# Kernel optimization log

Measured on AMD Instinct MI355X. Metric: run time of the kernel, lower is better.

## Reference

```python
import jax, jax.numpy as jnp
import numpy as np

GRID_SIZE = 5
SPLINE_ORDER = 3

def _grid():
    h = 2.0 / GRID_SIZE
    return jnp.arange(-SPLINE_ORDER, GRID_SIZE + SPLINE_ORDER + 1, dtype=jnp.float32) * h - 1.0

def b_splines(x):
    # x: (..., in) -> (..., in, GRID_SIZE + SPLINE_ORDER) Cox-de Boor bases on uniform grid [-1,1]
    g = _grid()
    x = x[..., None]
    bases = ((x >= g[:-1]) & (x < g[1:])).astype(x.dtype)
    for k in range(1, SPLINE_ORDER + 1):
        bases = ((x - g[:-(k + 1)]) / (g[k:-1] - g[:-(k + 1)]) * bases[..., :-1]
                 + (g[k + 1:] - x) / (g[k + 1:] - g[1:-k]) * bases[..., 1:])
    return bases

def kan(x, base_w, spline_w):
    # efficient-KAN KANLinear: silu(x) @ Wb^T + Bspline(x) contracted with Ws
    base = jax.nn.silu(x) @ base_w.T
    return base + jnp.einsum('...ik,oik->...o', b_splines(x), spline_w)

def token_mixing(X, ln_w, ln_b, k1b, k1s, k2b, k2s, eps=1e-5):
    # X: (B, C, L); LayerNorm over [L, C] jointly after permute, then KAN over last (token) dim
    z = jnp.transpose(X, (0, 2, 1))  # (B, L, C)
    mu = z.mean(axis=(-2, -1), keepdims=True)
    var = ((z - mu) ** 2).mean(axis=(-2, -1), keepdims=True)
    z = (z - mu) / jnp.sqrt(var + eps) * ln_w + ln_b
    z = jnp.transpose(z, (0, 2, 1))
    z = kan(z, k1b, k1s)
    z = kan(z, k2b, k2s)
    return X + z

def prob_distance(X, A):
    # Mahalanobis_mask.calculate_prob_distance
    XF = jnp.abs(jnp.fft.rfft(X, axis=-1))           # (B, C, F)
    diff = XF[:, :, None, :] - XF[:, None, :, :]     # (B, C, C, F)
    temp = jnp.einsum('dk,bxck->bxcd', A, diff)
    dist = jnp.einsum('bxcd,bxcd->bxc', temp, temp)
    exp_dist = 1.0 / (dist + 1e-10)
    C = exp_dist.shape[-1]
    eye = jnp.eye(C, dtype=exp_dist.dtype)
    off = 1.0 - eye
    exp_dist = exp_dist * off
    exp_max = jax.lax.stop_gradient(jnp.max(exp_dist, axis=-1, keepdims=True))
    p = exp_dist / exp_max
    return (p * off + eye) * 0.99

def gcn_spatial(x, a, w, b):
    # nconv spatial: einsum('bld,blw->bld', x, A) == x * A.sum(-1, keepdims); order=2, eval-mode dropout=identity
    s = jnp.sum(a, axis=-1, keepdims=True)  # (B, C, 1)
    x1 = x * s
    x2 = x1 * s
    h = jnp.concatenate([x, x1, x2], axis=-1) @ w.T + b
    return jax.nn.gelu(h, approximate=False)  # torch nn.GELU (erf)

def _forward(x, tm1_ln_w, tm1_ln_b, tm1_k1_base, tm1_k1_spline, tm1_k2_base, tm1_k2_spline, A1, g1_w, g1_b,
             k1_base, k1_spline, tm_ln_w, tm_ln_b, tm_k1_base, tm_k1_spline, tm_k2_base, tm_k2_spline, A2,
             g2_w, g2_b, k2_base, k2_spline):
    tm1 = token_mixing(x, tm1_ln_w, tm1_ln_b, tm1_k1_base, tm1_k1_spline, tm1_k2_base, tm1_k2_spline)
    P1 = prob_distance(tm1, A1)
    y1 = gcn_spatial(tm1, jax.nn.softmax(P1, axis=-1), g1_w, g1_b)
    cm = kan(x, k1_base, k1_spline)              # (B, C4, D)
    tm = token_mixing(cm, tm_ln_w, tm_ln_b, tm_k1_base, tm_k1_spline, tm_k2_base, tm_k2_spline)
    P3 = prob_distance(tm, A2)
    y2 = gcn_spatial(tm, jax.nn.softmax(P3, axis=-1), g2_w, g2_b)
    z = kan(y2, k2_base, k2_spline)              # (B, C4, T)
    return y1 + z

def setup_inputs() -> dict:
    key = jax.random.key(0)
    ks = jax.random.split(key, 20)
    B, T, D, C4, H, K = 16, 512, 512, 128, 64, GRID_SIZE + SPLINE_ORDER
    FT, FD = T // 2 + 1, D // 2 + 1
    r = lambda k, shape, s=0.05: jax.random.normal(k, shape, dtype=jnp.float32) * s
    return {
        'x': jax.random.normal(ks[0], (B, C4, T), dtype=jnp.float32),
        'tm1_ln_w': jnp.ones((T, C4), jnp.float32),
        'tm1_ln_b': jnp.zeros((T, C4), jnp.float32),
        'tm1_k1_base': r(ks[1], (H, T)),
        'tm1_k1_spline': r(ks[2], (H, T, K)),
        'tm1_k2_base': r(ks[3], (T, H)),
        'tm1_k2_spline': r(ks[4], (T, H, K)),
        'A1': jax.random.normal(ks[5], (FT, FT), dtype=jnp.float32),
        'g1_w': r(ks[6], (T, 3 * T), 0.02),
        'g1_b': jnp.zeros((T,), jnp.float32),
        'k1_base': r(ks[7], (D, T)),
        'k1_spline': r(ks[8], (D, T, K)),
        'tm_ln_w': jnp.ones((D, C4), jnp.float32),
        'tm_ln_b': jnp.zeros((D, C4), jnp.float32),
        'tm_k1_base': r(ks[9], (H, D)),
        'tm_k1_spline': r(ks[10], (H, D, K)),
        'tm_k2_base': r(ks[11], (D, H)),
        'tm_k2_spline': r(ks[12], (D, H, K)),
        'A2': jax.random.normal(ks[13], (FD, FD), dtype=jnp.float32),
        'g2_w': r(ks[14], (D, 3 * D), 0.02),
        'g2_b': jnp.zeros((D,), jnp.float32),
        'k2_base': r(ks[15], (T, D)),
        'k2_spline': r(ks[16], (T, D, K)),
    }

def reference(x, tm1_ln_w, tm1_ln_b, tm1_k1_base, tm1_k1_spline, tm1_k2_base, tm1_k2_spline, A1, g1_w, g1_b,
              k1_base, k1_spline, tm_ln_w, tm_ln_b, tm_k1_base, tm_k1_spline, tm_k2_base, tm_k2_spline, A2,
              g2_w, g2_b, k2_base, k2_spline):
    return _forward(x, tm1_ln_w, tm1_ln_b, tm1_k1_base, tm1_k1_spline, tm1_k2_base, tm1_k2_spline, A1, g1_w, g1_b,
                    k1_base, k1_spline, tm_ln_w, tm_ln_b, tm_k1_base, tm_k1_spline, tm_k2_base, tm_k2_spline, A2,
                    g2_w, g2_b, k2_base, k2_spline)
```

## Files before the change

### kernel.cpp

```cpp
#include <hip/hip_runtime.h>
#include <hip/hip_bf16.h>


#define M_ROWS 2048
#define TDIM   512
#define C4DIM  128
#define NFEAT  9
#define HZ     12
#define BZ     4

typedef unsigned short u16;
typedef __attribute__((ext_vector_type(8))) short short8;
typedef __attribute__((ext_vector_type(4))) float f32x4;

__device__ __forceinline__ float bf2f(u16 u) {
    union { unsigned int i; float f; } c; c.i = ((unsigned int)u) << 16; return c.f;
}
__device__ __forceinline__ u16 f2bf(float v) {
    __hip_bfloat16 h = __float2bfloat16(v);
    return *reinterpret_cast<u16*>(&h);
}
__device__ __forceinline__ float siluf(float v) { return v / (1.0f + __expf(-v)); }
__device__ __forceinline__ float geluf(float v) {
    return 0.5f * v * (1.0f + erff(v * 0.70710678118654752440f));
}
__device__ __forceinline__ void gload16(const void* g, void* l) {
    __builtin_amdgcn_global_load_lds(
        (const __attribute__((address_space(1))) unsigned int*)g,
        (__attribute__((address_space(3))) unsigned int*)l, 16, 0, 0);
}

__device__ __forceinline__ void features9(float v, float* f) {
    f[0] = siluf(v);
    float b[11];
#pragma unroll
    for (int i = 0; i < 11; ++i) {
        float gi  = (float)(i - 3) * 0.4f - 1.0f;
        float gi1 = (float)(i - 2) * 0.4f - 1.0f;
        b[i] = (v >= gi && v < gi1) ? 1.0f : 0.0f;
    }
#pragma unroll
    for (int k = 1; k <= 3; ++k) {
#pragma unroll
        for (int i = 0; i + k < 11; ++i) {
            float gi   = (float)(i - 3) * 0.4f - 1.0f;
            float gi1  = (float)(i - 2) * 0.4f - 1.0f;
            float gik  = (float)(i + k - 3) * 0.4f - 1.0f;
            float gik1 = (float)(i + k - 2) * 0.4f - 1.0f;
            b[i] = (v - gi) * (1.0f / (gik - gi)) * b[i]
                 + (gik1 - v) * (1.0f / (gik1 - gi1)) * b[i + 1];
        }
    }
#pragma unroll
    for (int k = 0; k < 8; ++k) f[1 + k] = b[k];
}

struct PrepPtrs {
    const float *g1_w, *g2_w;
    const float *b1, *s1, *b2, *s2, *b3, *s3, *b4, *s4, *b5, *s5, *b6, *s6;
    u16 *WE1, *WE2, *W1a, *W1b, *W2a, *W2b, *KX1, *KX2;
    const float *ln1w, *ln1b, *ln2w, *ln2b;
    float *LNT;
    float *SR;
};

__device__ __forceinline__ void wcat_one(const float* bw, const float* sw, u16* out,
                                         int idx, int I) {
    int o = idx / I, i = idx - o * I;
    u16* w = out + (size_t)o * NFEAT * I;
    w[i] = f2bf(bw[idx]);
    const float* sp = sw + (size_t)idx * 8;
#pragma unroll
    for (int k = 0; k < 8; ++k) w[(1 + k) * I + i] = f2bf(sp[k]);
}

__global__ void prep_all(PrepPtrs p) {
    int blk = blockIdx.x, tid = threadIdx.x;
    if (blk < 2048) {
        const float* gw = blk < 1024 ? p.g1_w : p.g2_w;
        u16* we = blk < 1024 ? p.WE1 : p.WE2;
        int idx = (blk & 1023) * 256 + tid;
        int o = idx >> 9, i = idx & 511;
        const float* r = gw + (size_t)o * 1536;
        we[idx] = f2bf(r[i] + r[512 + i] + r[1024 + i]);
    } else if (blk < 2560) {
        int sub = blk - 2048, which = sub >> 7;
        int idx = (sub & 127) * 256 + tid;
        if (which == 0)      wcat_one(p.b1, p.s1, p.W1a, idx, 512);
        else if (which == 1) wcat_one(p.b2, p.s2, p.W1b, idx, 512);
        else if (which == 2) wcat_one(p.b3, p.s3, p.W2a, idx, 64);
        else                 wcat_one(p.b4, p.s4, p.W2b, idx, 64);
    } else if (blk < 4608) {
        int sub = blk - 2560;
        int idx = (sub & 1023) * 256 + tid;
        if (sub < 1024) wcat_one(p.b5, p.s5, p.KX1, idx, 512);
        else            wcat_one(p.b6, p.s6, p.KX2, idx, 512);
    } else if (blk < 5632) {
        int sub = blk - 4608, which = sub >> 8;
        const float* src = which == 0 ? p.ln1w : which == 1 ? p.ln1b
                         : which == 2 ? p.ln2w : p.ln2b;
        float* dst = p.LNT + (size_t)which * 65536;
        int idx = (sub & 255) * 256 + tid;
        int c = idx & 127, l = idx >> 7;
        dst[c * 512 + l] = src[idx];
    } else {
        if (tid < 64) p.SR[tid] = 0.f;
    }
}

__global__ void stats1_convert(const float* __restrict__ X, u16* __restrict__ XB,
                               float* __restrict__ SR) {
    int idx = (blockIdx.x * 256 + threadIdx.x) * 4;
    float4 v = *reinterpret_cast<const float4*>(X + idx);
    ushort4 o; o.x = f2bf(v.x); o.y = f2bf(v.y); o.z = f2bf(v.z); o.w = f2bf(v.w);
    *reinterpret_cast<ushort4*>(XB + idx) = o;
    float s = v.x + v.y + v.z + v.w;
    float q = v.x * v.x + v.y * v.y + v.z * v.z + v.w * v.w;
#pragma unroll
    for (int off = 32; off > 0; off >>= 1) {
        s += __shfl_down(s, off);
        q += __shfl_down(q, off);
    }
    __shared__ float ls[4], lq[4];
    int wv = threadIdx.x >> 6;
    if ((threadIdx.x & 63) == 0) { ls[wv] = s; lq[wv] = q; }
    __syncthreads();
    if (threadIdx.x == 0) {
        s = ls[0] + ls[1] + ls[2] + ls[3];
        q = lq[0] + lq[1] + lq[2] + lq[3];
        int b = (blockIdx.x * 1024) >> 16;
        atomicAdd(&SR[b * 2], s);
        atomicAdd(&SR[b * 2 + 1], q);
    }
}

__global__ void reduce4_bf16_stats(const float* __restrict__ P, u16* __restrict__ out,
                                   float* __restrict__ SR) {
    int idx = (blockIdx.x * 256 + threadIdx.x) * 4;
    const size_t PL = (size_t)M_ROWS * 512;
    float4 sv = *reinterpret_cast<const float4*>(P + idx);
#pragma unroll
    for (int z = 1; z < BZ; ++z) {
        float4 t = *reinterpret_cast<const float4*>(P + z * PL + idx);
        sv.x += t.x; sv.y += t.y; sv.z += t.z; sv.w += t.w;
    }
    ushort4 o; o.x = f2bf(sv.x); o.y = f2bf(sv.y); o.z = f2bf(sv.z); o.w = f2bf(sv.w);
    *reinterpret_cast<ushort4*>(out + idx) = o;
    float s = sv.x + sv.y + sv.z + sv.w;
    float q = sv.x * sv.x + sv.y * sv.y + sv.z * sv.z + sv.w * sv.w;
#pragma unroll
    for (int off = 32; off > 0; off >>= 1) {
        s += __shfl_down(s, off);
        q += __shfl_down(q, off);
    }
    __shared__ float ls[4], lq[4];
    int wv = threadIdx.x >> 6;
    if ((threadIdx.x & 63) == 0) { ls[wv] = s; lq[wv] = q; }
    __syncthreads();
    if (threadIdx.x == 0) {
        s = ls[0] + ls[1] + ls[2] + ls[3];
        q = lq[0] + lq[1] + lq[2] + lq[3];
        int b = (blockIdx.x * 1024) >> 16;
        atomicAdd(&SR[b * 2], s);
        atomicAdd(&SR[b * 2 + 1], q);
    }
}


__global__ void build_feat_dual(const float* __restrict__ X, const float* __restrict__ SR,
                                const float* __restrict__ lnwT, const float* __restrict__ lnbT,
                                u16* __restrict__ FA, u16* __restrict__ FB) {
    int m = blockIdx.x;
    int i0 = threadIdx.x * 4;
    float4 xv = *reinterpret_cast<const float4*>(X + (size_t)m * TDIM + i0);
    int b = m >> 7, c = m & 127;
    float mu   = SR[b * 2] * (1.0f / 65536.0f);
    float var  = SR[b * 2 + 1] * (1.0f / 65536.0f) - mu * mu;
    float rstd = rsqrtf(var + 1e-5f);
    float4 lw = *reinterpret_cast<const float4*>(lnwT + (size_t)c * 512 + i0);
    float4 lb = *reinterpret_cast<const float4*>(lnbT + (size_t)c * 512 + i0);
    float fb[4][NFEAT], fa[4][NFEAT];
    float xe[4] = {xv.x, xv.y, xv.z, xv.w};
    float lwv[4] = {lw.x, lw.y, lw.z, lw.w};
    float lbv[4] = {lb.x, lb.y, lb.z, lb.w};
#pragma unroll
    for (int e = 0; e < 4; ++e) {
        features9(xe[e], fb[e]);
        features9((xe[e] - mu) * rstd * lwv[e] + lbv[e], fa[e]);
    }
    u16* oa = FA + (size_t)m * (NFEAT * TDIM) + i0;
    u16* ob = FB + (size_t)m * (NFEAT * TDIM) + i0;
#pragma unroll
    for (int j = 0; j < NFEAT; ++j) {
        ushort4 va, vb;
        va.x = f2bf(fa[0][j]); va.y = f2bf(fa[1][j]);
        va.z = f2bf(fa[2][j]); va.w = f2bf(fa[3][j]);
        vb.x = f2bf(fb[0][j]); vb.y = f2bf(fb[1][j]);
        vb.z = f2bf(fb[2][j]); vb.w = f2bf(fb[3][j]);
        *reinterpret_cast<ushort4*>(oa + j * TDIM) = va;
        *reinterpret_cast<ushort4*>(ob + j * TDIM) = vb;
    }
}

__global__ void build_feat_ln(const u16* __restrict__ X, const float* __restrict__ SR,
                              const float* __restrict__ lnwT, const float* __restrict__ lnbT,
                              u16* __restrict__ FA) {
    int m = blockIdx.x;
    int i0 = threadIdx.x * 4;
    ushort4 xu = *reinterpret_cast<const ushort4*>(X + (size_t)m * TDIM + i0);
    int b = m >> 7, c = m & 127;
    float mu   = SR[b * 2] * (1.0f / 65536.0f);
    float var  = SR[b * 2 + 1] * (1.0f / 65536.0f) - mu * mu;
    float rstd = rsqrtf(var + 1e-5f);
    float4 lw = *reinterpret_cast<const float4*>(lnwT + (size_t)c * 512 + i0);
    float4 lb = *reinterpret_cast<const float4*>(lnbT + (size_t)c * 512 + i0);
    float fa[4][NFEAT];
    float xe[4] = {bf2f(xu.x), bf2f(xu.y), bf2f(xu.z), bf2f(xu.w)};
    float lwv[4] = {lw.x, lw.y, lw.z, lw.w};
    float lbv[4] = {lb.x, lb.y, lb.z, lb.w};
#pragma unroll
    for (int e = 0; e < 4; ++e)
        features9((xe[e] - mu) * rstd * lwv[e] + lbv[e], fa[e]);
    u16* oa = FA + (size_t)m * (NFEAT * TDIM) + i0;
#pragma unroll
    for (int j = 0; j < NFEAT; ++j) {
        ushort4 va;
        va.x = f2bf(fa[0][j]); va.y = f2bf(fa[1][j]);
        va.z = f2bf(fa[2][j]); va.w = f2bf(fa[3][j]);
        *reinterpret_cast<ushort4*>(oa + j * TDIM) = va;
    }
}

__global__ void build_feat2(const float* __restrict__ PART, u16* __restrict__ FEAT2) {
    int idx = blockIdx.x * blockDim.x + threadIdx.x;
    int m = idx >> 6, i = idx & 63;
    float h = 0.f;
#pragma unroll
    for (int z = 0; z < HZ; ++z) h += PART[((size_t)z * M_ROWS + m) * 64 + i];
    float f[NFEAT];
    features9(h, f);
    u16* out = FEAT2 + (size_t)m * (NFEAT * 64) + i;
#pragma unroll
    for (int j = 0; j < NFEAT; ++j) out[j * 64] = f2bf(f[j]);
}

__global__ void reduce4_add(const float* __restrict__ P, float* __restrict__ out) {
    int idx = (blockIdx.x * 256 + threadIdx.x) * 4;
    const size_t PL = (size_t)M_ROWS * 512;
    float4 s = *reinterpret_cast<float4*>(out + idx);
#pragma unroll
    for (int z = 0; z < BZ; ++z) {
        float4 t = *reinterpret_cast<const float4*>(P + z * PL + idx);
        s.x += t.x; s.y += t.y; s.z += t.z; s.w += t.w;
    }
    *reinterpret_cast<float4*>(out + idx) = s;
}

__global__ __launch_bounds__(512)
void gemm_big(const u16* __restrict__ A, const u16* __restrict__ B,
              float* __restrict__ Cout) {
    constexpr int Kd = 4608, kPerZ = Kd / BZ, NT = 512;
    constexpr int nt = kPerZ / 64;
    __shared__ u16 As[2][64][64];
    __shared__ u16 Bs[2][128][64];

    const int lin = blockIdx.x;
    const int sw  = (lin & 7) * 64 + (lin >> 3);
    const int bn = (sw & 3) * 128;
    const int bm = ((sw >> 2) & 31) * 64;
    const int z  = sw >> 7;

    const int tid  = threadIdx.x;
    const int wave = tid >> 6, lane = tid & 63;
    const int wm = (wave >> 2) * 32, wn = (wave & 3) * 32;
    const int lr = lane & 15, kh = lane >> 4;

    const u16* Ab = A + (size_t)bm * Kd + z * kPerZ;
    const u16* Bb = B + (size_t)bn * Kd + z * kPerZ;

    const int l3  = lane >> 3;
    const int swz = ((lane & 7) ^ l3) * 8;

    f32x4 acc[2][2];
#pragma unroll
    for (int a = 0; a < 2; ++a)
#pragma unroll
        for (int b = 0; b < 2; ++b) acc[a][b] = (f32x4){0.f, 0.f, 0.f, 0.f};

#define BIG_ISSUE(buf, kt)                                                         \
    {                                                                              \
        _Pragma("unroll")                                                          \
        for (int c = 0; c < 3; ++c) {                                              \
            int cc = wave * 3 + c;                                                 \
            if (cc < 8) {                                                          \
                int row = cc * 8 + l3;                                             \
                gload16(Ab + (size_t)row * Kd + (kt) + swz, &As[buf][cc * 8][0]);  \
            } else {                                                               \
                int row = (cc - 8) * 8 + l3;                                       \
                gload16(Bb + (size_t)row * Kd + (kt) + swz, &Bs[buf][(cc - 8) * 8][0]); \
            }                                                                      \
        }                                                                          \
    }

    BIG_ISSUE(0, 0);
    int cur = 0;
    for (int t = 0; t < nt; ++t) {
        __syncthreads();
        if (t + 1 < nt) BIG_ISSUE(cur ^ 1, (t + 1) * 64);
#pragma unroll
        for (int ks = 0; ks < 2; ++ks) {
            short8 af[2], bfr[2];
#pragma unroll
            for (int a = 0; a < 2; ++a) {
                int row = wm + a * 16 + lr;
                af[a] = *reinterpret_cast<const short8*>(
                    &As[cur][row][((ks * 4 + kh) ^ (lr & 7)) * 8]);
            }
#pragma unroll
            for (int b = 0; b < 2; ++b) {
                int row = wn + b * 16 + lr;
                bfr[b] = *reinterpret_cast<const short8*>(
                    &Bs[cur][row][((ks * 4 + kh) ^ (lr & 7)) * 8]);
            }
#pragma unroll
            for (int a = 0; a < 2; ++a)
#pragma unroll
                for (int b = 0; b < 2; ++b)
                    acc[a][b] = __builtin_amdgcn_mfma_f32_16x16x32_bf16(af[a], bfr[b], acc[a][b], 0, 0, 0);
        }
        cur ^= 1;
    }

    const int r0 = kh * 4;
#pragma unroll
    for (int a = 0; a < 2; ++a)
#pragma unroll
        for (int b = 0; b < 2; ++b)
#pragma unroll
            for (int r = 0; r < 4; ++r) {
                int row = bm + wm + a * 16 + r0 + r;
                int col = bn + wn + b * 16 + lr;
                Cout[((size_t)z * M_ROWS + row) * NT + col] = acc[a][b][r];
            }
}

template<int BM, int BN, int EPI, bool OUTF32>
__global__ __launch_bounds__(256)
void gemm_mfma(const u16* __restrict__ A, const u16* __restrict__ B,
               void* __restrict__ Cout, const void* __restrict__ aux,
               int M, int N, int Kd, int kPerZ) {
    constexpr int WSM = BM / 2, WSN = BN / 2;
    constexpr int FM = WSM / 16, FN = WSN / 16;
    constexpr int CA = BM / 32, CB = BN / 32;
    __shared__ u16 As[BM][72];
    __shared__ u16 Bs[BN][72];

    const int tid  = threadIdx.x;
    const int wave = tid >> 6, lane = tid & 63;
    const int wm = (wave >> 1) * WSM, wn = (wave & 1) * WSN;
    const int lr = lane & 15, kh = lane >> 4;
    const int bm = blockIdx.y * BM, bn = blockIdx.x * BN;
    const int k0 = blockIdx.z * kPerZ;
    const int nt = kPerZ >> 6;

    const u16* Ab = A + (size_t)bm * Kd + k0;
    const u16* Bb = B + (size_t)bn * Kd + k0;

    f32x4 acc[FM][FN];
#pragma unroll
    for (int a = 0; a < FM; ++a)
#pragma unroll
        for (int b = 0; b < FN; ++b) acc[a][b] = (f32x4){0.f, 0.f, 0.f, 0.f};

    uint4 arA[CA], brA[CB], arB[CA], brB[CB];

#define GLOADT(ar, br, kt)                                                          \
    {                                                                               \
        _Pragma("unroll")                                                           \
        for (int c = 0; c < CA; ++c) {                                              \
            int id = tid + c * 256;                                                 \
            ar[c] = *reinterpret_cast<const uint4*>(Ab + (size_t)(id >> 3) * Kd + (kt) + (id & 7) * 8); \
        }                                                                           \
        _Pragma("unroll")                                                           \
        for (int c = 0; c < CB; ++c) {                                              \
            int id = tid + c * 256;                                                 \
            br[c] = *reinterpret_cast<const uint4*>(Bb + (size_t)(id >> 3) * Kd + (kt) + (id & 7) * 8); \
        }                                                                           \
    }
#define GWRITET(ar, br)                                                             \
    {                                                                               \
        _Pragma("unroll")                                                           \
        for (int c = 0; c < CA; ++c) {                                              \
            int id = tid + c * 256;                                                 \
            *reinterpret_cast<uint4*>(&As[id >> 3][(id & 7) * 8]) = ar[c];          \
        }                                                                           \
        _Pragma("unroll")                                                           \
        for (int c = 0; c < CB; ++c) {                                              \
            int id = tid + c * 256;                                                 \
            *reinterpret_cast<uint4*>(&Bs[id >> 3][(id & 7) * 8]) = br[c];          \
        }                                                                           \
    }
#define GMFMAT()                                                                    \
    {                                                                               \
        _Pragma("unroll")                                                           \
        for (int ks = 0; ks < 2; ++ks) {                                            \
            short8 af[FM], bfr[FN];                                                 \
            _Pragma("unroll")                                                       \
            for (int a = 0; a < FM; ++a)                                            \
                af[a] = *reinterpret_cast<const short8*>(&As[wm + a * 16 + lr][ks * 32 + kh * 8]); \
            _Pragma("unroll")                                                       \
            for (int b = 0; b < FN; ++b)                                            \
                bfr[b] = *reinterpret_cast<const short8*>(&Bs[wn + b * 16 + lr][ks * 32 + kh * 8]); \
            _Pragma("unroll")                                                       \
            for (int a = 0; a < FM; ++a)                                            \
                _Pragma("unroll")                                                   \
                for (int b = 0; b < FN; ++b)                                        \
                    acc[a][b] = __builtin_amdgcn_mfma_f32_16x16x32_bf16(af[a], bfr[b], acc[a][b], 0, 0, 0); \
        }                                                                           \
    }

    GLOADT(arA, brA, 0);
    if (nt > 1) GLOADT(arB, brB, 64);
    int t = 0;
    for (; t + 1 < nt; t += 2) {
        __syncthreads();
        GWRITET(arA, brA);
        __syncthreads();
        if (t + 2 < nt) GLOADT(arA, brA, (t + 2) * 64);
        GMFMAT();
        __syncthreads();
        GWRITET(arB, brB);
        __syncthreads();
        if (t + 3 < nt) GLOADT(arB, brB, (t + 3) * 64);
        GMFMAT();
    }
    if (t < nt) {
        __syncthreads();
        GWRITET(arA, brA);
        __syncthreads();
        GMFMAT();
    }

    const int r0 = kh * 4;
#pragma unroll
    for (int a = 0; a < FM; ++a) {
#pragma unroll
        for (int b = 0; b < FN; ++b) {
#pragma unroll
            for (int r = 0; r < 4; ++r) {
                int row = bm + wm + a * 16 + r0 + r;
                int col = bn + wn + b * 16 + lr;
                float v = acc[a][b][r];
                if (EPI == 0) {
                    ((float*)Cout)[((size_t)blockIdx.z * M + row) * N + col] = v;
                } else if (EPI == 1) {
                    v += bf2f(((const u16*)aux)[(size_t)row * N + col]);
                    ((u16*)Cout)[(size_t)row * N + col] = f2bf(v);
                } else if (EPI == 2) {
                    v = geluf(v + ((const float*)aux)[col]);
                    if (OUTF32) ((float*)Cout)[(size_t)row * N + col] = v;
                    else        ((u16*)Cout)[(size_t)row * N + col] = f2bf(v);
                } else {
                    v = geluf(v + ((const float*)aux)[col]);
                    float f[NFEAT];
                    features9(v, f);
                    u16* o = (u16*)Cout + (size_t)row * (NFEAT * TDIM) + col;
#pragma unroll
                    for (int j = 0; j < NFEAT; ++j) o[j * TDIM] = f2bf(f[j]);
                }
            }
        }
    }
}

extern "C" void kernel_launch(void* const* d_in, const int* in_sizes, int n_in,
                              void* d_out, int out_size, void* d_ws, size_t ws_size,
                              hipStream_t stream) {
    const float* x            = (const float*)d_in[0];
    const float* tm1_ln_w     = (const float*)d_in[1];
    const float* tm1_ln_b     = (const float*)d_in[2];
    const float* tm1_k1_base  = (const float*)d_in[3];
    const float* tm1_k1_spl   = (const float*)d_in[4];
    const float* tm1_k2_base  = (const float*)d_in[5];
    const float* tm1_k2_spl   = (const float*)d_in[6];
    const float* g1_w         = (const float*)d_in[8];
    const float* g1_b         = (const float*)d_in[9];
    const float* k1_base      = (const float*)d_in[10];
    const float* k1_spl       = (const float*)d_in[11];
    const float* tm_ln_w      = (const float*)d_in[12];
    const float* tm_ln_b      = (const float*)d_in[13];
    const float* tm_k1_base   = (const float*)d_in[14];
    const float* tm_k1_spl    = (const float*)d_in[15];
    const float* tm_k2_base   = (const float*)d_in[16];
    const float* tm_k2_spl    = (const float*)d_in[17];
    const float* g2_w         = (const float*)d_in[19];
    const float* g2_b         = (const float*)d_in[20];
    const float* k2_base      = (const float*)d_in[21];
    const float* k2_spl       = (const float*)d_in[22];

    float* out = (float*)d_out;

    char* w = (char*)d_ws;
    u16*   FEATA = (u16*)w;   w += (size_t)M_ROWS * 4608 * 2;
    u16*   FEATB = (u16*)w;   w += (size_t)M_ROWS * 4608 * 2;
    u16*   FEAT2 = (u16*)w;   w += (size_t)M_ROWS * 576 * 2;
    float* PART  = (float*)w; w += (size_t)BZ * M_ROWS * 512 * 4;
    u16*   XB    = (u16*)w;   w += (size_t)M_ROWS * 512 * 2;
    u16*   BUF1  = (u16*)w;   w += (size_t)M_ROWS * 512 * 2;
    u16*   BUF2  = (u16*)w;   w += (size_t)M_ROWS * 512 * 2;
    u16*   W1a   = (u16*)w;   w += (size_t)64 * 4608 * 2;
    u16*   W1b   = (u16*)w;   w += (size_t)64 * 4608 * 2;
    u16*   W2a   = (u16*)w;   w += (size_t)512 * 576 * 2;
    u16*   W2b   = (u16*)w;   w += (size_t)512 * 576 * 2;
    u16*   WE1   = (u16*)w;   w += (size_t)512 * 512 * 2;
    u16*   WE2   = (u16*)w;   w += (size_t)512 * 512 * 2;
    u16*   KX1   = (u16*)w;   w += (size_t)512 * 4608 * 2;
    u16*   KX2   = (u16*)w;   w += (size_t)512 * 4608 * 2;
    float* LNT   = (float*)w; w += (size_t)4 * 65536 * 4;
    float* SR    = (float*)w; w += 64 * 4;
    const float* LNT0w = LNT, *LNT0b = LNT + 65536;
    const float* LNT2w = LNT + 131072, *LNT2b = LNT + 196608;

    PrepPtrs p;
    p.g1_w = g1_w; p.g2_w = g2_w;
    p.b1 = tm1_k1_base; p.s1 = tm1_k1_spl;
    p.b2 = tm_k1_base;  p.s2 = tm_k1_spl;
    p.b3 = tm1_k2_base; p.s3 = tm1_k2_spl;
    p.b4 = tm_k2_base;  p.s4 = tm_k2_spl;
    p.b5 = k1_base;     p.s5 = k1_spl;
    p.b6 = k2_base;     p.s6 = k2_spl;
    p.WE1 = WE1; p.WE2 = WE2; p.W1a = W1a; p.W1b = W1b;
    p.W2a = W2a; p.W2b = W2b; p.KX1 = KX1; p.KX2 = KX2;
    p.ln1w = tm1_ln_w; p.ln1b = tm1_ln_b; p.ln2w = tm_ln_w; p.ln2b = tm_ln_b;
    p.LNT = LNT; p.SR = SR;
    prep_all<<<5633, 256, 0, stream>>>(p);

    stats1_convert<<<1024, 256, 0, stream>>>(x, XB, SR);
    build_feat_dual<<<M_ROWS, 128, 0, stream>>>(x, SR, LNT0w, LNT0b, FEATA, FEATB);

    gemm_mfma<64, 64, 0, true><<<dim3(1, 32, HZ), 256, 0, stream>>>(FEATA, W1a, PART, nullptr, M_ROWS, 64, 4608, 4608 / HZ);
    build_feat2<<<512, 256, 0, stream>>>(PART, FEAT2);
    gemm_mfma<64, 32, 1, false><<<dim3(16, 32, 1), 256, 0, stream>>>(FEAT2, W2a, BUF1, XB, M_ROWS, 512, 576, 576);
    gemm_mfma<64, 32, 2, true><<<dim3(16, 32, 1), 256, 0, stream>>>(BUF1, WE1, out, g1_b, M_ROWS, 512, 512, 512);

    gemm_big<<<512, 512, 0, stream>>>(FEATB, KX1, PART);
    reduce4_bf16_stats<<<1024, 256, 0, stream>>>(PART, BUF2, SR + 32);

    build_feat_ln<<<M_ROWS, 128, 0, stream>>>(BUF2, SR + 32, LNT2w, LNT2b, FEATA);
    gemm_mfma<64, 64, 0, true><<<dim3(1, 32, HZ), 256, 0, stream>>>(FEATA, W1b, PART, nullptr, M_ROWS, 64, 4608, 4608 / HZ);
    build_feat2<<<512, 256, 0, stream>>>(PART, FEAT2);
    gemm_mfma<64, 32, 1, false><<<dim3(16, 32, 1), 256, 0, stream>>>(FEAT2, W2b, BUF1, BUF2, M_ROWS, 512, 576, 576);
    gemm_mfma<64, 32, 3, false><<<dim3(16, 32, 1), 256, 0, stream>>>(BUF1, WE2, FEATB, g2_b, M_ROWS, 512, 512, 512);

    gemm_big<<<512, 512, 0, stream>>>(FEATB, KX2, PART);
    reduce4_add<<<1024, 256, 0, stream>>>(PART, out);
}
```

Before: 332.3 us.

## Replace register-staged GEMM loads with direct-to-LDS async loads and XOR swizzle

The small MFMA GEMM kernel now issues global-to-LDS direct loads (gload16, presumably already used by gemm_big) into a double-buffered shared tile, replacing the register-staged load/write scheme. The LDS layout drops the 72-element padding and uses an XOR swizzle on 8-element chunks to avoid bank conflicts. The goal is to remove the VGPR round trip and one barrier per tile, and to overlap the next tile's load with the current MFMAs. It relies on the async load being complete by the next __syncthreads, and hardcodes 32 rows per wave, so BM must be 64.

```diff
diff --git a/kernel.cpp b/kernel.cpp
--- a/kernel.cpp
+++ b/kernel.cpp
@@ -346,18 +346,18 @@
 
 template<int BM, int BN, int EPI, bool OUTF32>
 __global__ __launch_bounds__(256)
-void gemm_mfma(const u16* __restrict__ A, const u16* __restrict__ B,
-               void* __restrict__ Cout, const void* __restrict__ aux,
-               int M, int N, int Kd, int kPerZ) {
-    constexpr int WSM = BM / 2, WSN = BN / 2;
-    constexpr int FM = WSM / 16, FN = WSN / 16;
-    constexpr int CA = BM / 32, CB = BN / 32;
-    __shared__ u16 As[BM][72];
-    __shared__ u16 Bs[BN][72];
+void gemm_dma(const u16* __restrict__ A, const u16* __restrict__ B,
+              void* __restrict__ Cout, const void* __restrict__ aux,
+              int M, int N, int Kd, int kPerZ) {
+    constexpr int NCA = BM / 8, NCB = BN / 8, NCH = NCA + NCB;
+    constexpr int CPW = NCH / 4;
+    constexpr int FN = BN / 32;
+    __shared__ u16 As[2][BM][64];
+    __shared__ u16 Bs[2][BN][64];
 
     const int tid  = threadIdx.x;
     const int wave = tid >> 6, lane = tid & 63;
-    const int wm = (wave >> 1) * WSM, wn = (wave & 1) * WSN;
+    const int wm = (wave >> 1) * 32, wn = (wave & 1) * (BN / 2);
     const int lr = lane & 15, kh = lane >> 4;
     const int bm = blockIdx.y * BM, bn = blockIdx.x * BN;
     const int k0 = blockIdx.z * kPerZ;
@@ -366,84 +366,62 @@
     const u16* Ab = A + (size_t)bm * Kd + k0;
     const u16* Bb = B + (size_t)bn * Kd + k0;
 
-    f32x4 acc[FM][FN];
-#pragma unroll
-    for (int a = 0; a < FM; ++a)
+    const int l3  = lane >> 3;
+    const int swz = ((lane & 7) ^ l3) * 8;
+
+    f32x4 acc[2][FN];
+#pragma unroll
+    for (int a = 0; a < 2; ++a)
 #pragma unroll
         for (int b = 0; b < FN; ++b) acc[a][b] = (f32x4){0.f, 0.f, 0.f, 0.f};
 
-    uint4 arA[CA], brA[CB], arB[CA], brB[CB];
-
-#define GLOADT(ar, br, kt)                                                          \
-    {                                                                               \
-        _Pragma("unroll")                                                           \
-        for (int c = 0; c < CA; ++c) {                                              \
-            int id = tid + c * 256;                                                 \
-            ar[c] = *reinterpret_cast<const uint4*>(Ab + (size_t)(id >> 3) * Kd + (kt) + (id & 7) * 8); \
-        }                                                                           \
-        _Pragma("unroll")                                                           \
-        for (int c = 0; c < CB; ++c) {                                              \
-            int id = tid + c * 256;                                                 \
-            br[c] = *reinterpret_cast<const uint4*>(Bb + (size_t)(id >> 3) * Kd + (kt) + (id & 7) * 8); \
-        }                                                                           \
-    }
-#define GWRITET(ar, br)                                                             \
-    {                                                                               \
-        _Pragma("unroll")                                                           \
-        for (int c = 0; c < CA; ++c) {                                              \
-            int id = tid + c * 256;                                                 \
-            *reinterpret_cast<uint4*>(&As[id >> 3][(id & 7) * 8]) = ar[c];          \
-        }                                                                           \
-        _Pragma("unroll")                                                           \
-        for (int c = 0; c < CB; ++c) {                                              \
-            int id = tid + c * 256;                                                 \
-            *reinterpret_cast<uint4*>(&Bs[id >> 3][(id & 7) * 8]) = br[c];          \
-        }                                                                           \
-    }
-#define GMFMAT()                                                                    \
-    {                                                                               \
-        _Pragma("unroll")                                                           \
-        for (int ks = 0; ks < 2; ++ks) {                                            \
-            short8 af[FM], bfr[FN];                                                 \
-            _Pragma("unroll")                                                       \
-            for (int a = 0; a < FM; ++a)                                            \
-                af[a] = *reinterpret_cast<const short8*>(&As[wm + a * 16 + lr][ks * 32 + kh * 8]); \
-            _Pragma("unroll")                                                       \
-            for (int b = 0; b < FN; ++b)                                            \
-                bfr[b] = *reinterpret_cast<const short8*>(&Bs[wn + b * 16 + lr][ks * 32 + kh * 8]); \
-            _Pragma("unroll")                                                       \
-            for (int a = 0; a < FM; ++a)                                            \
-                _Pragma("unroll")                                                   \
-                for (int b = 0; b < FN; ++b)                                        \
-                    acc[a][b] = __builtin_amdgcn_mfma_f32_16x16x32_bf16(af[a], bfr[b], acc[a][b], 0, 0, 0); \
-        }                                                                           \
-    }
-
-    GLOADT(arA, brA, 0);
-    if (nt > 1) GLOADT(arB, brB, 64);
-    int t = 0;
-    for (; t + 1 < nt; t += 2) {
+#define DMA_ISSUE(buf, kt)                                                         \
+    {                                                                              \
+        _Pragma("unroll")                                                          \
+        for (int c = 0; c < CPW; ++c) {                                            \
+            int cc = wave * CPW + c;                                               \
+            if (cc < NCA) {                                                        \
+                int row = cc * 8 + l3;                                             \
+                gload16(Ab + (size_t)row * Kd + (kt) + swz, &As[buf][cc * 8][0]);  \
+            } else {                                                               \
+                int row = (cc - NCA) * 8 + l3;                                     \
+                gload16(Bb + (size_t)row * Kd + (kt) + swz, &Bs[buf][(cc - NCA) * 8][0]); \
+            }                                                                      \
+        }                                                                          \
+    }
+
+    DMA_ISSUE(0, 0);
+    int cur = 0;
+    for (int t = 0; t < nt; ++t) {
         __syncthreads();
-        GWRITET(arA, brA);
-        __syncthreads();
-        if (t + 2 < nt) GLOADT(arA, brA, (t + 2) * 64);
-        GMFMAT();
-        __syncthreads();
-        GWRITET(arB, brB);
-        __syncthreads();
-        if (t + 3 < nt) GLOADT(arB, brB, (t + 3) * 64);
-        GMFMAT();
-    }
-    if (t < nt) {
-        __syncthreads();
-        GWRITET(arA, brA);
-        __syncthreads();
-        GMFMAT();
+        if (t + 1 < nt) DMA_ISSUE(cur ^ 1, (t + 1) * 64);
+#pragma unroll
+        for (int ks = 0; ks < 2; ++ks) {
+            short8 af[2], bfr[FN];
+#pragma unroll
+            for (int a = 0; a < 2; ++a) {
+                int row = wm + a * 16 + lr;
+                af[a] = *reinterpret_cast<const short8*>(
+                    &As[cur][row][((ks * 4 + kh) ^ (lr & 7)) * 8]);
+            }
+#pragma unroll
+            for (int b = 0; b < FN; ++b) {
+                int row = wn + b * 16 + lr;
+                bfr[b] = *reinterpret_cast<const short8*>(
+                    &Bs[cur][row][((ks * 4 + kh) ^ (lr & 7)) * 8]);
+            }
+#pragma unroll
+            for (int a = 0; a < 2; ++a)
+#pragma unroll
+                for (int b = 0; b < FN; ++b)
+                    acc[a][b] = __builtin_amdgcn_mfma_f32_16x16x32_bf16(af[a], bfr[b], acc[a][b], 0, 0, 0);
+        }
+        cur ^= 1;
     }
 
     const int r0 = kh * 4;
 #pragma unroll
-    for (int a = 0; a < FM; ++a) {
+    for (int a = 0; a < 2; ++a) {
 #pragma unroll
         for (int b = 0; b < FN; ++b) {
 #pragma unroll
@@ -538,19 +516,19 @@
     stats1_convert<<<1024, 256, 0, stream>>>(x, XB, SR);
     build_feat_dual<<<M_ROWS, 128, 0, stream>>>(x, SR, LNT0w, LNT0b, FEATA, FEATB);
 
-    gemm_mfma<64, 64, 0, true><<<dim3(1, 32, HZ), 256, 0, stream>>>(FEATA, W1a, PART, nullptr, M_ROWS, 64, 4608, 4608 / HZ);
+    gemm_dma<64, 64, 0, true><<<dim3(1, 32, HZ), 256, 0, stream>>>(FEATA, W1a, PART, nullptr, M_ROWS, 64, 4608, 4608 / HZ);
     build_feat2<<<512, 256, 0, stream>>>(PART, FEAT2);
-    gemm_mfma<64, 32, 1, false><<<dim3(16, 32, 1), 256, 0, stream>>>(FEAT2, W2a, BUF1, XB, M_ROWS, 512, 576, 576);
-    gemm_mfma<64, 32, 2, true><<<dim3(16, 32, 1), 256, 0, stream>>>(BUF1, WE1, out, g1_b, M_ROWS, 512, 512, 512);
+    gemm_dma<64, 32, 1, false><<<dim3(16, 32, 1), 256, 0, stream>>>(FEAT2, W2a, BUF1, XB, M_ROWS, 512, 576, 576);
+    gemm_dma<64, 32, 2, true><<<dim3(16, 32, 1), 256, 0, stream>>>(BUF1, WE1, out, g1_b, M_ROWS, 512, 512, 512);
 
     gemm_big<<<512, 512, 0, stream>>>(FEATB, KX1, PART);
     reduce4_bf16_stats<<<1024, 256, 0, stream>>>(PART, BUF2, SR + 32);
 
     build_feat_ln<<<M_ROWS, 128, 0, stream>>>(BUF2, SR + 32, LNT2w, LNT2b, FEATA);
-    gemm_mfma<64, 64, 0, true><<<dim3(1, 32, HZ), 256, 0, stream>>>(FEATA, W1b, PART, nullptr, M_ROWS, 64, 4608, 4608 / HZ);
+    gemm_dma<64, 64, 0, true><<<dim3(1, 32, HZ), 256, 0, stream>>>(FEATA, W1b, PART, nullptr, M_ROWS, 64, 4608, 4608 / HZ);
     build_feat2<<<512, 256, 0, stream>>>(PART, FEAT2);
-    gemm_mfma<64, 32, 1, false><<<dim3(16, 32, 1), 256, 0, stream>>>(FEAT2, W2b, BUF1, BUF2, M_ROWS, 512, 576, 576);
-    gemm_mfma<64, 32, 3, false><<<dim3(16, 32, 1), 256, 0, stream>>>(BUF1, WE2, FEATB, g2_b, M_ROWS, 512, 512, 512);
+    gemm_dma<64, 32, 1, false><<<dim3(16, 32, 1), 256, 0, stream>>>(FEAT2, W2b, BUF1, BUF2, M_ROWS, 512, 576, 576);
+    gemm_dma<64, 32, 3, false><<<dim3(16, 32, 1), 256, 0, stream>>>(BUF1, WE2, FEATB, g2_b, M_ROWS, 512, 512, 512);
 
     gemm_big<<<512, 512, 0, stream>>>(FEATB, KX2, PART);
     reduce4_add<<<1024, 256, 0, stream>>>(PART, out);
```

Result: faster. 278.6 us (-16.2%).
